# Optimization experiments

Hardware: AMD Instinct MI355X
Metric: run time of the kernel (lower is better)

The kernel has to match this reference:

```python
import jax, jax.numpy as jnp
import numpy as np


def setup_inputs() -> dict:
    key = jax.random.key(0)
    k1, k2 = jax.random.split(key)
    x = jax.random.normal(k1, (4, 4096, 128), dtype=jnp.float32)
    kernel = jax.random.normal(k2, (3, 128, 64), dtype=jnp.float32)
    return {"x": x, "kernel": kernel}


def reference(x, kernel):
    # QKV projections: x [B,N,Din] @ kernel[i] [Din,Dout] -> [B,N,Dout]
    WQ = jnp.einsum('bnd,de->bne', x, kernel[0])
    WK = jnp.einsum('bnd,de->bne', x, kernel[1])
    WV = jnp.einsum('bnd,de->bne', x, kernel[2])
    d_out = WV.shape[-1]
    # scaled dot-product scores [B,N,N]
    scores = jnp.einsum('bqe,bke->bqk', WQ, WK) / jnp.sqrt(jnp.float32(d_out))
    attn = jax.nn.softmax(scores, axis=-1)
    return jnp.einsum('bqk,bke->bqe', attn, WV)
```

## Files before the change

### kernel.cpp

```cpp
#include <hip/hip_runtime.h>


typedef __attribute__((ext_vector_type(8))) short bf16x8;
typedef __attribute__((ext_vector_type(16))) float f32x16;
typedef __attribute__((ext_vector_type(4))) unsigned u32x4;
typedef unsigned short us;

__device__ __forceinline__ us f2bf(float f) {
  unsigned u = __builtin_bit_cast(unsigned, f);
  u += 0x7FFFu + ((u >> 16) & 1u);
  return (us)(u >> 16);
}
__device__ __forceinline__ float bf2f(us h) {
  unsigned u = ((unsigned)h) << 16;
  return __builtin_bit_cast(float, u);
}
__device__ __forceinline__ f32x16 mfma(bf16x8 a, bf16x8 b, f32x16 c) {
  return __builtin_amdgcn_mfma_f32_32x32x16_bf16(a, b, c, 0, 0, 0);
}
__device__ __forceinline__ unsigned pk2t(float a, float b) {
  return __builtin_amdgcn_perm(__builtin_bit_cast(unsigned, b),
                               __builtin_bit_cast(unsigned, a), 0x07060302u);
}
#define EXP2(x) __builtin_amdgcn_exp2f(x)

__device__ __forceinline__ void gld16(const us* g, us* l) {
  __builtin_amdgcn_global_load_lds(
      (__attribute__((address_space(1))) const unsigned int*)g,
      (__attribute__((address_space(3))) unsigned int*)l, 16, 0, 0);
}

#define NSEG 8
#define ITERS 8

__global__ __launch_bounds__(256, 1) void wprep_kernel(
    const float* __restrict__ w, us* __restrict__ Wbh, us* __restrict__ Wbl)
{
  const int i = blockIdx.x * 256 + threadIdx.x;
  if (i >= 24576) return;
  const int p = i >> 13, d = (i & 8191) >> 6, e = i & 63;
  float v = w[i];
  if (p == 0) v *= 0.18033688011112042f;
  const us hi = f2bf(v);
  const us lo = f2bf(v - bf2f(hi));
  const int g = (p * 64 + e) >> 5, ks = d >> 4, hh = (d >> 3) & 1, j = d & 7;
  const int o = ((g * 8 + ks) * 2 + hh) * 256 + (e & 31) * 8 + j;
  Wbh[o] = hi;
  Wbl[o] = lo;
}

__global__ __launch_bounds__(384, 1) void qkv_kernel(
    const float* __restrict__ x,
    const us* __restrict__ Wbh, const us* __restrict__ Wbl,
    us* __restrict__ Qhi, us* __restrict__ Qlo,
    us* __restrict__ Khi, us* __restrict__ Klo, us* __restrict__ Vb)
{
  __shared__ unsigned ttile[32 * 193];
  const int t = threadIdx.x;
  const int rb = blockIdx.x;
  const int wid = t >> 6, lane = t & 63;
  const int l31 = lane & 31, h = lane >> 5;
  const int rbase = rb * 32;
  const float* xrow = x + (size_t)(rbase + l31) * 128;

  f32x16 acc = {};
  #pragma unroll
  for (int ks = 0; ks < 8; ++ks) {
    const int d0 = ks * 16 + h * 8;
    const float4 xa = *(const float4*)(xrow + d0);
    const float4 xb = *(const float4*)(xrow + d0 + 4);
    const float xv[8] = {xa.x, xa.y, xa.z, xa.w, xb.x, xb.y, xb.z, xb.w};
    bf16x8 ah, al;
    #pragma unroll
    for (int j = 0; j < 8; ++j) {
      us hi = f2bf(xv[j]);
      ah[j] = (short)hi;
      al[j] = (short)f2bf(xv[j] - bf2f(hi));
    }
    const int wo = ((wid * 8 + ks) * 2 + h) * 256 + l31 * 8;
    bf16x8 bh = *(const bf16x8*)(Wbh + wo);
    bf16x8 bl = *(const bf16x8*)(Wbl + wo);
    acc = mfma(ah, bh, acc);
    acc = mfma(al, bh, acc);
    acc = mfma(ah, bl, acc);
  }

  #pragma unroll
  for (int r = 0; r < 16; ++r) {
    const int rl = (r & 3) + 8 * (r >> 2) + 4 * h;
    float v = acc[r];
    us hi = f2bf(v);
    us lo = f2bf(v - bf2f(hi));
    ttile[rl * 193 + wid * 32 + l31] = (unsigned)hi | ((unsigned)lo << 16);
  }
  __syncthreads();

  if (t < 64) {
    const int row = t >> 1, cb = (t & 1) * 32;
    const int grow = rbase + row;
    unsigned hw[16], lw[16];
    #pragma unroll
    for (int j = 0; j < 16; ++j) {
      unsigned a = ttile[row * 193 + cb + 2 * j];
      unsigned bv = ttile[row * 193 + cb + 2 * j + 1];
      hw[j] = (a & 0xffffu) | (bv << 16);
      lw[j] = (a >> 16) | (bv & 0xffff0000u);
    }
    #pragma unroll
    for (int j = 0; j < 4; ++j) {
      uint4 hv = {hw[4 * j], hw[4 * j + 1], hw[4 * j + 2], hw[4 * j + 3]};
      uint4 lv = {lw[4 * j], lw[4 * j + 1], lw[4 * j + 2], lw[4 * j + 3]};
      *(uint4*)(Qhi + (size_t)grow * 64 + cb + 8 * j) = hv;
      *(uint4*)(Qlo + (size_t)grow * 64 + cb + 8 * j) = lv;
    }
  } else if (t < 192) {
    const int tt = t - 64;
    const int row = tt >> 2, cs = (tt & 3) * 16;
    const int grow = rbase + row;
    unsigned hw[8], lw[8];
    #pragma unroll
    for (int j = 0; j < 8; ++j) {
      unsigned a = ttile[row * 193 + 64 + cs + 2 * j];
      unsigned bv = ttile[row * 193 + 64 + cs + 2 * j + 1];
      hw[j] = (a & 0xffffu) | (bv << 16);
      lw[j] = (a >> 16) | (bv & 0xffff0000u);
    }
    #pragma unroll
    for (int j = 0; j < 2; ++j) {
      uint4 hv = {hw[4 * j], hw[4 * j + 1], hw[4 * j + 2], hw[4 * j + 3]};
      uint4 lv = {lw[4 * j], lw[4 * j + 1], lw[4 * j + 2], lw[4 * j + 3]};
      *(uint4*)(Khi + (size_t)grow * 64 + cs + 8 * j) = hv;
      *(uint4*)(Klo + (size_t)grow * 64 + cs + 8 * j) = lv;
    }
  } else if (t < 320) {
    const int bb = rbase >> 12;
    const int nb = rbase & 4095;
    #pragma unroll
    for (int i2 = 0; i2 < 2; ++i2) {
      const int c = (t - 192) + 128 * i2;
      const int e = c >> 2, nc = c & 3;
      unsigned p[4];
      #pragma unroll
      for (int j = 0; j < 4; ++j) {
        unsigned a = ttile[(nc * 8 + 2 * j) * 193 + 128 + e];
        unsigned bv = ttile[(nc * 8 + 2 * j + 1) * 193 + 128 + e];
        p[j] = (a & 0xffffu) | (bv << 16);
      }
      uint4 pv = {p[0], p[1], p[2], p[3]};
      const int n0 = nb + nc * 8;
      const int kt = n0 >> 6, sub = n0 & 63;
      const int ks = sub >> 4, hh = (sub >> 3) & 1;
      const int dt = e >> 5, lv = e & 31;
      *(uint4*)(Vb + (size_t)bb * 262144 +
                ((((kt * 4 + ks) * 2 + hh) * 2 + dt) * 256 + lv * 8)) = pv;
    }
  }
}

__global__ __launch_bounds__(256, 3) void attn_kernel(
    const us* __restrict__ Qhi, const us* __restrict__ Qlo,
    const us* __restrict__ Khi, const us* __restrict__ Klo,
    const us* __restrict__ Vb,
    us* __restrict__ Opart, float* __restrict__ Mpart,
    float* __restrict__ Lpart)
{
  __shared__ union {
    struct {
      us k[2][2][4096];
      us v[2][4096];
    } tl;
    float fb[4][2112];
  } sm;
  __shared__ float alds[4][32];

  const int bx = blockIdx.x;
  const int xc = bx & 7, b = xc >> 1;
  const int idx = ((bx >> 3) << 1) | (xc & 1);
  const int seg = idx & (NSEG - 1), qg = idx >> 3;
  const int t = threadIdx.x;
  const int wid = t >> 6, lane = t & 63;
  const int l31 = lane & 31, h = lane >> 5;
  const int q0 = qg * 128 + wid * 32;
  const int u = (b * 4096 + q0) >> 5;
  const size_t pb = (size_t)u * NSEG + seg;

  bf16x8 qh[4], ql[4];
  {
    const size_t rg = (size_t)(b * 4096 + q0 + l31) * 64;
    #pragma unroll
    for (int ks = 0; ks < 4; ++ks) {
      qh[ks] = *(const bf16x8*)(Qhi + rg + ks * 16 + h * 8);
      ql[ks] = *(const bf16x8*)(Qlo + rg + ks * 16 + h * 8);
    }
  }
  const size_t kbase = (size_t)b * 262144;
  const size_t vbb = (size_t)b * 262144;

  const int row0 = t >> 3, slot = t & 7;
  const int gcol = (slot ^ (row0 & 7)) * 8;
  const int wb = 512 * wid;
  const int vw0 = (wid * 2) * 512;
  const int vw1 = (wid * 2 + 1) * 512;

  {
    const int k0 = seg * 512;
    gld16(Khi + kbase + (size_t)(k0 + row0) * 64 + gcol, &sm.tl.k[0][0][wb]);
    gld16(Khi + kbase + (size_t)(k0 + row0 + 32) * 64 + gcol, &sm.tl.k[0][0][wb + 2048]);
    gld16(Klo + kbase + (size_t)(k0 + row0) * 64 + gcol, &sm.tl.k[0][1][wb]);
    gld16(Klo + kbase + (size_t)(k0 + row0 + 32) * 64 + gcol, &sm.tl.k[0][1][wb + 2048]);
    const size_t vt = vbb + (size_t)(seg * ITERS) * 4096;
    gld16(Vb + vt + vw0 + lane * 8, &sm.tl.v[0][vw0]);
    gld16(Vb + vt + vw1 + lane * 8, &sm.tl.v[0][vw1]);
  }
  __syncthreads();

  f32x16 o[2] = {};
  float mrun = -__builtin_inff();
  float lrun = 0.f;

  for (int it = 0; it < ITERS; ++it) {
    const int cur = it & 1, nxt = cur ^ 1;
    const int KT = seg * ITERS + it;

    if (it + 1 < ITERS) {
      const int nk = (KT + 1) * 64;
      gld16(Khi + kbase + (size_t)(nk + row0) * 64 + gcol, &sm.tl.k[nxt][0][wb]);
      gld16(Khi + kbase + (size_t)(nk + row0 + 32) * 64 + gcol, &sm.tl.k[nxt][0][wb + 2048]);
      gld16(Klo + kbase + (size_t)(nk + row0) * 64 + gcol, &sm.tl.k[nxt][1][wb]);
      gld16(Klo + kbase + (size_t)(nk + row0 + 32) * 64 + gcol, &sm.tl.k[nxt][1][wb + 2048]);
      const size_t vt = vbb + (size_t)(KT + 1) * 4096;
      gld16(Vb + vt + vw0 + lane * 8, &sm.tl.v[nxt][vw0]);
      gld16(Vb + vt + vw1 + lane * 8, &sm.tl.v[nxt][vw1]);
    }

    f32x16 s[2] = {};
    #pragma unroll
    for (int m = 0; m < 2; ++m) {
      const int krow = 32 * m + l31;
      #pragma unroll
      for (int ks = 0; ks < 4; ++ks) {
        const int off = krow * 64 + (((2 * ks + h) ^ (l31 & 7)) * 8);
        bf16x8 ah = *(const bf16x8*)(&sm.tl.k[cur][0][off]);
        bf16x8 al = *(const bf16x8*)(&sm.tl.k[cur][1][off]);
        s[m] = mfma(ah, qh[ks], s[m]);
        s[m] = mfma(al, qh[ks], s[m]);
        s[m] = mfma(ah, ql[ks], s[m]);
      }
    }

    float vm = -__builtin_inff();
    #pragma unroll
    for (int r = 0; r < 16; ++r)
      vm = fmaxf(vm, fmaxf(s[0][r], s[1][r]));
    vm = fmaxf(vm, __shfl_xor(vm, 32));

    if (!__all(vm <= mrun - 24.f)) {
      const float mnew = (vm > mrun + 0.5f) ? vm : mrun;
      const float alpha = EXP2(mrun - mnew);
      float sum = 0.f;
      unsigned pp[2][8];
      #pragma unroll
      for (int m = 0; m < 2; ++m) {
        #pragma unroll
        for (int p = 0; p < 8; ++p) {
          const float p0 = EXP2(s[m][2 * p] - mnew);
          const float p1 = EXP2(s[m][2 * p + 1] - mnew);
          sum += p0 + p1;
          pp[m][p] = pk2t(p0, p1);
        }
      }
      sum += __shfl_xor(sum, 32);
      lrun = lrun * alpha + sum;
      mrun = mnew;

      if (__any(alpha != 1.f)) {
        if (!h) alds[wid][l31] = alpha;
        #pragma unroll
        for (int g = 0; g < 4; ++g) {
          const float4 af4 = *(const float4*)(&alds[wid][8 * g + 4 * h]);
          #pragma unroll
          for (int rr = 0; rr < 4; ++rr) {
            const int r = 4 * g + rr;
            const float a = (rr == 0) ? af4.x : (rr == 1) ? af4.y
                           : (rr == 2) ? af4.z : af4.w;
            o[0][r] *= a;
            o[1][r] *= a;
          }
        }
      }

      #pragma unroll
      for (int ks = 0; ks < 4; ++ks) {
        const int m = ks >> 1, base = 4 * (ks & 1);
        const unsigned x0 = pp[m][base + 0], x1 = pp[m][base + 1];
        const unsigned x2 = pp[m][base + 2], x3 = pp[m][base + 3];
        const unsigned sA = h ? x0 : x2;
        const unsigned sB = h ? x1 : x3;
        const unsigned rA = (unsigned)__shfl_xor((int)sA, 32);
        const unsigned rB = (unsigned)__shfl_xor((int)sB, 32);
        u32x4 wv;
        wv.x = h ? rA : x0;
        wv.y = h ? rB : x1;
        wv.z = h ? x2 : rA;
        wv.w = h ? x3 : rB;
        const bf16x8 af = __builtin_bit_cast(bf16x8, wv);
        const int vo = ((2 * ks + h) * 2) * 256 + l31 * 8;
        const bf16x8 vf0 = *(const bf16x8*)(&sm.tl.v[cur][vo]);
        const bf16x8 vf1 = *(const bf16x8*)(&sm.tl.v[cur][vo + 256]);
        o[0] = mfma(af, vf0, o[0]);
        o[1] = mfma(af, vf1, o[1]);
      }
    }

    __syncthreads();
  }

  float* fb = sm.fb[wid];
  #pragma unroll
  for (int dt = 0; dt < 2; ++dt) {
    #pragma unroll
    for (int r = 0; r < 16; ++r) {
      const int qrow = (r & 3) + 8 * (r >> 2) + 4 * h;
      fb[qrow * 66 + l31 + 32 * dt] = o[dt][r];
    }
  }
  #pragma unroll
  for (int jj = 0; jj < 4; ++jj) {
    const int chunk = lane + 64 * jj;
    const int rw = chunk >> 3, part = chunk & 7;
    const float* src = &fb[rw * 66 + part * 8];
    float2 a0 = *(const float2*)(src + 0);
    float2 a1 = *(const float2*)(src + 2);
    float2 a2 = *(const float2*)(src + 4);
    float2 a3 = *(const float2*)(src + 6);
    uint4 pkv;
    pkv.x = pk2t(a0.x, a0.y);
    pkv.y = pk2t(a1.x, a1.y);
    pkv.z = pk2t(a2.x, a2.y);
    pkv.w = pk2t(a3.x, a3.y);
    *(uint4*)(Opart + pb * 2048 + (size_t)rw * 64 + part * 8) = pkv;
  }
  if (!h) {
    Mpart[pb * 32 + l31] = mrun;
    Lpart[pb * 32 + l31] = lrun;
  }
}

__global__ __launch_bounds__(256, 1) void merge_kernel(
    const us* __restrict__ Opart, const float* __restrict__ Mpart,
    const float* __restrict__ Lpart, float* __restrict__ out)
{
  const int tg = blockIdx.x * 256 + threadIdx.x;
  const int q = tg >> 3, dc = (tg & 7) * 8;
  const int u = q >> 5, ql = q & 31;
  const int base = u * NSEG;
  float M = -__builtin_inff();
  #pragma unroll
  for (int s = 0; s < NSEG; ++s)
    M = fmaxf(M, Mpart[(size_t)(base + s) * 32 + ql]);
  float acc[8] = {};
  float den = 0.f;
  #pragma unroll
  for (int s = 0; s < NSEG; ++s) {
    const float wgt = EXP2(Mpart[(size_t)(base + s) * 32 + ql] - M);
    den += wgt * Lpart[(size_t)(base + s) * 32 + ql];
    const uint4 r = *(const uint4*)(Opart + (size_t)(base + s) * 2048 +
                                    ql * 64 + dc);
    const unsigned rw[4] = {r.x, r.y, r.z, r.w};
    #pragma unroll
    for (int j = 0; j < 4; ++j) {
      acc[2 * j]     += wgt * bf2f((us)(rw[j] & 0xffffu));
      acc[2 * j + 1] += wgt * bf2f((us)(rw[j] >> 16));
    }
  }
  const float inv = 1.f / den;
  float4 r0 = {acc[0] * inv, acc[1] * inv, acc[2] * inv, acc[3] * inv};
  float4 r1 = {acc[4] * inv, acc[5] * inv, acc[6] * inv, acc[7] * inv};
  *(float4*)(out + (size_t)q * 64 + dc) = r0;
  *(float4*)(out + (size_t)q * 64 + dc + 4) = r1;
}

extern "C" void kernel_launch(void* const* d_in, const int* in_sizes, int n_in,
                              void* d_out, int out_size, void* d_ws,
                              size_t ws_size, hipStream_t stream)
{
  const float* x = (const float*)d_in[0];
  const float* w = (const float*)d_in[1];
  float* out = (float*)d_out;
  char* ws = (char*)d_ws;

  const size_t T = 2097152;
  us* Qhi = (us*)(ws + 0 * T);
  us* Qlo = (us*)(ws + 1 * T);
  us* Khi = (us*)(ws + 2 * T);
  us* Klo = (us*)(ws + 3 * T);
  us* Vb  = (us*)(ws + 4 * T);
  us* Wbh = (us*)(ws + 5 * T);
  us* Wbl = (us*)(ws + 5 * T + 49152);
  char* pbase = ws + 5 * T + 98304;
  us* Opart = (us*)pbase;
  float* Mpart = (float*)(pbase + 16777216);
  float* Lpart = (float*)(pbase + 16777216 + 524288);

  hipLaunchKernelGGL(wprep_kernel, dim3(96), dim3(256), 0, stream,
                     w, Wbh, Wbl);
  hipLaunchKernelGGL(qkv_kernel, dim3(512), dim3(384), 0, stream,
                     x, Wbh, Wbl, Qhi, Qlo, Khi, Klo, Vb);
  hipLaunchKernelGGL(attn_kernel, dim3(1024), dim3(256), 0, stream,
                     Qhi, Qlo, Khi, Klo, Vb, Opart, Mpart, Lpart);
  hipLaunchKernelGGL(merge_kernel, dim3(512), dim3(256), 0, stream,
                     Opart, Mpart, Lpart, out);
}
```

Baseline: 140.9 us.

## Load K and V fragments directly from global memory in MFMA layout, drop LDS staging

The QKV kernel now writes K hi/lo in a pre-swizzled fragment layout that matches the MFMA operand order. The attention kernel then reads K and V fragments straight from global memory into registers, replacing the double-buffered LDS tiles, global_load_lds prefetch and per-iteration barriers. This removes LDS traffic and synchronisation and lowers LDS use, but each of the four waves now fetches the same K/V tile separately. Load latency is no longer hidden by explicit prefetch, so it relies on L2/L1 hits and on the compiler scheduling the loads.

```diff
diff --git a/kernel.cpp b/kernel.cpp
--- a/kernel.cpp
+++ b/kernel.cpp
@@ -23,12 +23,6 @@
                                __builtin_bit_cast(unsigned, a), 0x07060302u);
 }
 #define EXP2(x) __builtin_amdgcn_exp2f(x)
-
-__device__ __forceinline__ void gld16(const us* g, us* l) {
-  __builtin_amdgcn_global_load_lds(
-      (__attribute__((address_space(1))) const unsigned int*)g,
-      (__attribute__((address_space(3))) unsigned int*)l, 16, 0, 0);
-}
 
 #define NSEG 8
 #define ITERS 8
@@ -53,7 +47,7 @@
     const float* __restrict__ x,
     const us* __restrict__ Wbh, const us* __restrict__ Wbl,
     us* __restrict__ Qhi, us* __restrict__ Qlo,
-    us* __restrict__ Khi, us* __restrict__ Klo, us* __restrict__ Vb)
+    us* __restrict__ Kbh, us* __restrict__ Kbl, us* __restrict__ Vb)
 {
   __shared__ unsigned ttile[32 * 193];
   const int t = threadIdx.x;
@@ -114,23 +108,27 @@
       *(uint4*)(Qlo + (size_t)grow * 64 + cb + 8 * j) = lv;
     }
   } else if (t < 192) {
-    const int tt = t - 64;
-    const int row = tt >> 2, cs = (tt & 3) * 16;
-    const int grow = rbase + row;
-    unsigned hw[8], lw[8];
-    #pragma unroll
-    for (int j = 0; j < 8; ++j) {
-      unsigned a = ttile[row * 193 + 64 + cs + 2 * j];
-      unsigned bv = ttile[row * 193 + 64 + cs + 2 * j + 1];
-      hw[j] = (a & 0xffffu) | (bv << 16);
-      lw[j] = (a >> 16) | (bv & 0xffff0000u);
-    }
-    #pragma unroll
-    for (int j = 0; j < 2; ++j) {
-      uint4 hv = {hw[4 * j], hw[4 * j + 1], hw[4 * j + 2], hw[4 * j + 3]};
-      uint4 lv = {lw[4 * j], lw[4 * j + 1], lw[4 * j + 2], lw[4 * j + 3]};
-      *(uint4*)(Khi + (size_t)grow * 64 + cs + 8 * j) = hv;
-      *(uint4*)(Klo + (size_t)grow * 64 + cs + 8 * j) = lv;
+    const int bb = rbase >> 12;
+    const int kt = (rbase & 4095) >> 6;
+    const int m = (rbase >> 5) & 1;
+    const size_t kbb = (size_t)bb * 262144 + (size_t)kt * 4096 + m * 256;
+    #pragma unroll
+    for (int i2 = 0; i2 < 2; ++i2) {
+      const int c = (t - 64) + 128 * i2;
+      const int r = c & 31, hh = (c >> 5) & 1, ks = c >> 6;
+      unsigned hw[4], lw[4];
+      #pragma unroll
+      for (int j = 0; j < 4; ++j) {
+        unsigned a = ttile[r * 193 + 64 + 16 * ks + 8 * hh + 2 * j];
+        unsigned bv = ttile[r * 193 + 64 + 16 * ks + 8 * hh + 2 * j + 1];
+        hw[j] = (a & 0xffffu) | (bv << 16);
+        lw[j] = (a >> 16) | (bv & 0xffff0000u);
+      }
+      const size_t off = kbb + (size_t)(ks * 4 + 2 * hh) * 256 + r * 8;
+      uint4 hv = {hw[0], hw[1], hw[2], hw[3]};
+      uint4 lv = {lw[0], lw[1], lw[2], lw[3]};
+      *(uint4*)(Kbh + off) = hv;
+      *(uint4*)(Kbl + off) = lv;
     }
   } else if (t < 320) {
     const int bb = rbase >> 12;
@@ -159,18 +157,12 @@
 
 __global__ __launch_bounds__(256, 3) void attn_kernel(
     const us* __restrict__ Qhi, const us* __restrict__ Qlo,
-    const us* __restrict__ Khi, const us* __restrict__ Klo,
+    const us* __restrict__ Kbh, const us* __restrict__ Kbl,
     const us* __restrict__ Vb,
     us* __restrict__ Opart, float* __restrict__ Mpart,
     float* __restrict__ Lpart)
 {
-  __shared__ union {
-    struct {
-      us k[2][2][4096];
-      us v[2][4096];
-    } tl;
-    float fb[4][2112];
-  } sm;
+  __shared__ float fb[4][2112];
   __shared__ float alds[4][32];
 
   const int bx = blockIdx.x;
@@ -194,58 +186,40 @@
     }
   }
   const size_t kbase = (size_t)b * 262144;
-  const size_t vbb = (size_t)b * 262144;
-
-  const int row0 = t >> 3, slot = t & 7;
-  const int gcol = (slot ^ (row0 & 7)) * 8;
-  const int wb = 512 * wid;
-  const int vw0 = (wid * 2) * 512;
-  const int vw1 = (wid * 2 + 1) * 512;
-
-  {
-    const int k0 = seg * 512;
-    gld16(Khi + kbase + (size_t)(k0 + row0) * 64 + gcol, &sm.tl.k[0][0][wb]);
-    gld16(Khi + kbase + (size_t)(k0 + row0 + 32) * 64 + gcol, &sm.tl.k[0][0][wb + 2048]);
-    gld16(Klo + kbase + (size_t)(k0 + row0) * 64 + gcol, &sm.tl.k[0][1][wb]);
-    gld16(Klo + kbase + (size_t)(k0 + row0 + 32) * 64 + gcol, &sm.tl.k[0][1][wb + 2048]);
-    const size_t vt = vbb + (size_t)(seg * ITERS) * 4096;
-    gld16(Vb + vt + vw0 + lane * 8, &sm.tl.v[0][vw0]);
-    gld16(Vb + vt + vw1 + lane * 8, &sm.tl.v[0][vw1]);
-  }
-  __syncthreads();
 
   f32x16 o[2] = {};
   float mrun = -__builtin_inff();
   float lrun = 0.f;
 
   for (int it = 0; it < ITERS; ++it) {
-    const int cur = it & 1, nxt = cur ^ 1;
     const int KT = seg * ITERS + it;
-
-    if (it + 1 < ITERS) {
-      const int nk = (KT + 1) * 64;
-      gld16(Khi + kbase + (size_t)(nk + row0) * 64 + gcol, &sm.tl.k[nxt][0][wb]);
-      gld16(Khi + kbase + (size_t)(nk + row0 + 32) * 64 + gcol, &sm.tl.k[nxt][0][wb + 2048]);
-      gld16(Klo + kbase + (size_t)(nk + row0) * 64 + gcol, &sm.tl.k[nxt][1][wb]);
-      gld16(Klo + kbase + (size_t)(nk + row0 + 32) * 64 + gcol, &sm.tl.k[nxt][1][wb + 2048]);
-      const size_t vt = vbb + (size_t)(KT + 1) * 4096;
-      gld16(Vb + vt + vw0 + lane * 8, &sm.tl.v[nxt][vw0]);
-      gld16(Vb + vt + vw1 + lane * 8, &sm.tl.v[nxt][vw1]);
-    }
+    const size_t tb = kbase + (size_t)KT * 4096;
 
     f32x16 s[2] = {};
     #pragma unroll
     for (int m = 0; m < 2; ++m) {
-      const int krow = 32 * m + l31;
+      bf16x8 ah[4], al[4];
       #pragma unroll
       for (int ks = 0; ks < 4; ++ks) {
-        const int off = krow * 64 + (((2 * ks + h) ^ (l31 & 7)) * 8);
-        bf16x8 ah = *(const bf16x8*)(&sm.tl.k[cur][0][off]);
-        bf16x8 al = *(const bf16x8*)(&sm.tl.k[cur][1][off]);
-        s[m] = mfma(ah, qh[ks], s[m]);
-        s[m] = mfma(al, qh[ks], s[m]);
-        s[m] = mfma(ah, ql[ks], s[m]);
-      }
+        const size_t ko = tb + (size_t)(ks * 4 + 2 * h + m) * 256 + l31 * 8;
+        ah[ks] = *(const bf16x8*)(Kbh + ko);
+        al[ks] = *(const bf16x8*)(Kbl + ko);
+      }
+      #pragma unroll
+      for (int ks = 0; ks < 4; ++ks) {
+        s[m] = mfma(ah[ks], qh[ks], s[m]);
+        s[m] = mfma(al[ks], qh[ks], s[m]);
+        s[m] = mfma(ah[ks], ql[ks], s[m]);
+      }
+    }
+
+    bf16x8 vf0[4], vf1[4];
+    #pragma unroll
+    for (int ks = 0; ks < 4; ++ks) {
+      const size_t vo = kbase + (size_t)(((KT * 4 + ks) * 2 + h) * 2) * 256 +
+                        l31 * 8;
+      vf0[ks] = *(const bf16x8*)(Vb + vo);
+      vf1[ks] = *(const bf16x8*)(Vb + vo + 256);
     }
 
     float vm = -__builtin_inff();
@@ -304,31 +278,26 @@
         wv.z = h ? x2 : rA;
         wv.w = h ? x3 : rB;
         const bf16x8 af = __builtin_bit_cast(bf16x8, wv);
-        const int vo = ((2 * ks + h) * 2) * 256 + l31 * 8;
-        const bf16x8 vf0 = *(const bf16x8*)(&sm.tl.v[cur][vo]);
-        const bf16x8 vf1 = *(const bf16x8*)(&sm.tl.v[cur][vo + 256]);
-        o[0] = mfma(af, vf0, o[0]);
-        o[1] = mfma(af, vf1, o[1]);
-      }
-    }
-
-    __syncthreads();
-  }
-
-  float* fb = sm.fb[wid];
+        o[0] = mfma(af, vf0[ks], o[0]);
+        o[1] = mfma(af, vf1[ks], o[1]);
+      }
+    }
+  }
+
+  float* fw = fb[wid];
   #pragma unroll
   for (int dt = 0; dt < 2; ++dt) {
     #pragma unroll
     for (int r = 0; r < 16; ++r) {
       const int qrow = (r & 3) + 8 * (r >> 2) + 4 * h;
-      fb[qrow * 66 + l31 + 32 * dt] = o[dt][r];
+      fw[qrow * 66 + l31 + 32 * dt] = o[dt][r];
     }
   }
   #pragma unroll
   for (int jj = 0; jj < 4; ++jj) {
     const int chunk = lane + 64 * jj;
     const int rw = chunk >> 3, part = chunk & 7;
-    const float* src = &fb[rw * 66 + part * 8];
+    const float* src = &fw[rw * 66 + part * 8];
     float2 a0 = *(const float2*)(src + 0);
     float2 a1 = *(const float2*)(src + 2);
     float2 a2 = *(const float2*)(src + 4);
@@ -392,8 +361,8 @@
   const size_t T = 2097152;
   us* Qhi = (us*)(ws + 0 * T);
   us* Qlo = (us*)(ws + 1 * T);
-  us* Khi = (us*)(ws + 2 * T);
-  us* Klo = (us*)(ws + 3 * T);
+  us* Kbh = (us*)(ws + 2 * T);
+  us* Kbl = (us*)(ws + 3 * T);
   us* Vb  = (us*)(ws + 4 * T);
   us* Wbh = (us*)(ws + 5 * T);
   us* Wbl = (us*)(ws + 5 * T + 49152);
@@ -405,9 +374,9 @@
   hipLaunchKernelGGL(wprep_kernel, dim3(96), dim3(256), 0, stream,
                      w, Wbh, Wbl);
   hipLaunchKernelGGL(qkv_kernel, dim3(512), dim3(384), 0, stream,
-                     x, Wbh, Wbl, Qhi, Qlo, Khi, Klo, Vb);
+                     x, Wbh, Wbl, Qhi, Qlo, Kbh, Kbl, Vb);
   hipLaunchKernelGGL(attn_kernel, dim3(1024), dim3(256), 0, stream,
-                     Qhi, Qlo, Khi, Klo, Vb, Opart, Mpart, Lpart);
+                     Qhi, Qlo, Kbh, Kbl, Vb, Opart, Mpart, Lpart);
   hipLaunchKernelGGL(merge_kernel, dim3(512), dim3(256), 0, stream,
                      Opart, Mpart, Lpart, out);
 }
```

New measurement: 127.2 us. -9.7%, faster.
